# Kernel tuning notes

Measured on AMD Instinct MI355X. Metric: run time of the kernel, lower is better.

## Reference

```python
import jax, jax.numpy as jnp
import numpy as np

N, D, H, O, P = 50000, 256, 512, 64, 1024


def setup_inputs() -> dict:
    key = jax.random.key(0)
    ks = jax.random.split(key, 9)
    x = jax.random.normal(ks[0], (N, D), dtype=jnp.float32)
    W1 = jax.random.normal(ks[1], (H, D), dtype=jnp.float32) / np.sqrt(D)
    b1 = jax.random.normal(ks[2], (H,), dtype=jnp.float32) * 0.01
    W2 = jax.random.normal(ks[3], (O, H), dtype=jnp.float32) / np.sqrt(H)
    b2 = jax.random.normal(ks[4], (O,), dtype=jnp.float32) * 0.01
    ap = jax.random.randint(ks[5], (P,), 0, N, dtype=jnp.int32)
    p = jax.random.randint(ks[6], (P,), 0, N, dtype=jnp.int32)
    an = jax.random.randint(ks[7], (P,), 0, N, dtype=jnp.int32)
    n = jax.random.randint(ks[8], (P,), 0, N, dtype=jnp.int32)
    return {"x": x, "W1": W1, "b1": b1, "W2": W2, "b2": b2,
            "ap": ap, "p": p, "an": an, "n": n}


def reference(x, W1, b1, W2, b2, ap, p, an, n):
    """ContrastiveHessianCalculator.compute_hessian, loss_func='contrastive_full',
    wrt='weight', shape='diagonal', speed='half' (exact GGN diag), for the nnj net
    Linear(D,H) -> Tanh -> Linear(H,O).

    For a pair (x1,x2) the combined diag m0 - 2*m1 + m2 equals
    diag((J1-J2)^T (J1-J2)) where Ji = d f(xi)/d params. Closed form per layer:
      W1[i,j]: S11_i*x1_j^2 - 2*S12_i*x1_j*x2_j + S22_i*x2_j^2,
               Sab_i = tanh'(z1a)_i * tanh'(z1b)_i * sum_o W2[o,i]^2
      b1[i]:   S11_i - 2*S12_i + S22_i
      W2[i,j]: (h1_j - h2_j)^2  (independent of output row i)
      b2[i]:   0  (bias Jacobians of the two branches cancel)
    Per-layer diags are flattened [weight, bias] and concatenated (torch.cat(.., dim=1)),
    then summed over the pair batch; return sum(pos) - sum(neg).
    """
    c = jnp.sum(W2 * W2, axis=0)  # [H]

    def pair_hess_diag(ia, ib):
        xa = x[ia]            # [P, D]
        xb = x[ib]            # [P, D]
        ha = jnp.tanh(xa @ W1.T + b1)   # [P, H]
        hb = jnp.tanh(xb @ W1.T + b1)
        da = 1.0 - ha * ha              # tanh' at x_a, [P, H]
        db = 1.0 - hb * hb
        S11 = da * da * c               # [P, H]
        S12 = da * db * c
        S22 = db * db * c
        # W1 diag: [P, H, D]
        W1d = (S11[:, :, None] * (xa * xa)[:, None, :]
               - 2.0 * S12[:, :, None] * (xa * xb)[:, None, :]
               + S22[:, :, None] * (xb * xb)[:, None, :])
        b1d = S11 - 2.0 * S12 + S22      # [P, H]
        hd = (ha - hb) ** 2              # [P, H]
        W2d = jnp.broadcast_to(hd[:, None, :], (hd.shape[0], O, H))  # [P, O, H]
        b2d = jnp.zeros((hd.shape[0], O), dtype=hd.dtype)
        flat = jnp.concatenate([W1d.reshape(hd.shape[0], -1), b1d,
                                W2d.reshape(hd.shape[0], -1), b2d], axis=1)
        return jnp.sum(flat, axis=0)     # sum over pair batch -> [n_params]

    pos = pair_hess_diag(ap, p)
    neg = pair_hess_diag(an, n)
    return pos - neg
```

## Files before the change

kernel.cpp:

```cpp
#include <hip/hip_runtime.h>
#include <math.h>

#define DD_ 256
#define HH_ 512
#define OO_ 64

typedef __attribute__((ext_vector_type(8))) short bf16x8s;
typedef __attribute__((ext_vector_type(4))) float f32x4;

__device__ __forceinline__ unsigned short f2bf(float f) {
    unsigned u = __float_as_uint(f);
    u += 0x7FFF + ((u >> 16) & 1);
    return (unsigned short)(u >> 16);
}
__device__ __forceinline__ float bf2f(unsigned short h) {
    return __uint_as_float(((unsigned)h) << 16);
}
__device__ __forceinline__ int swz4(int r, int g) {
    return g ^ (r & 3) ^ ((r >> 2) & 3);
}

__global__ __launch_bounds__(256) void k_mega(
    const float* __restrict__ x, const float* __restrict__ W1,
    const float* __restrict__ b1, const float* __restrict__ W2,
    const int* __restrict__ ap, const int* __restrict__ pI,
    const int* __restrict__ an, const int* __restrict__ nI,
    short* __restrict__ Mt, short* __restrict__ Xt,
    float* __restrict__ pb1, float* __restrict__ phd) {
    const int t = threadIdx.x;
    const int bb = blockIdx.x;
    if (bb < 512) {
        __shared__ short Ah[64 * 32], Al[64 * 32], Bh[64 * 32], Bl[64 * 32];
        __shared__ float ht[64][67];
        __shared__ int sidx[64];
        const int n0 = (bb & 7) * 64;
        const int ry = bb >> 3;
        const int s = ry >> 5;
        const int p0 = (ry & 31) * 32;
        const int* IA = s ? an : ap;
        const int* IB = s ? nI : pI;
        if (t < 32) sidx[t] = IA[p0 + t];
        else if (t < 64) sidx[t] = IB[p0 + t - 32];
        __syncthreads();
        const int row = t >> 2, q = t & 3;
        const int l = t & 63, w = t >> 6;
        const int wm = w >> 1, wn = w & 1;
        const int lm = l & 15, g = l >> 4;
        const int sw = swz4(row, q);
        f32x4 acc[2][2] = {};
        for (int k0 = 0; k0 < DD_; k0 += 32) {
            {
                const float* src = x + (size_t)sidx[row] * DD_ + k0 + q * 8;
                float4 v0 = *(const float4*)src;
                float4 v1 = *(const float4*)(src + 4);
                float f[8] = {v0.x, v0.y, v0.z, v0.w, v1.x, v1.y, v1.z, v1.w};
                bf16x8s hi, lo;
                #pragma unroll
                for (int e = 0; e < 8; ++e) {
                    unsigned short hh = f2bf(f[e]);
                    hi[e] = (short)hh;
                    lo[e] = (short)f2bf(f[e] - bf2f(hh));
                }
                *(bf16x8s*)(&Ah[(row * 4 + sw) * 8]) = hi;
                *(bf16x8s*)(&Al[(row * 4 + sw) * 8]) = lo;
            }
            {
                const float* src = W1 + (size_t)(n0 + row) * DD_ + k0 + q * 8;
                float4 v0 = *(const float4*)src;
                float4 v1 = *(const float4*)(src + 4);
                float f[8] = {v0.x, v0.y, v0.z, v0.w, v1.x, v1.y, v1.z, v1.w};
                bf16x8s hi, lo;
                #pragma unroll
                for (int e = 0; e < 8; ++e) {
                    unsigned short hh = f2bf(f[e]);
                    hi[e] = (short)hh;
                    lo[e] = (short)f2bf(f[e] - bf2f(hh));
                }
                *(bf16x8s*)(&Bh[(row * 4 + sw) * 8]) = hi;
                *(bf16x8s*)(&Bl[(row * 4 + sw) * 8]) = lo;
            }
            __syncthreads();
            bf16x8s ah[2], al[2], bh[2], bl[2];
            #pragma unroll
            for (int mi = 0; mi < 2; ++mi) {
                int r = wm * 32 + mi * 16 + lm;
                ah[mi] = *(const bf16x8s*)(&Ah[(r * 4 + swz4(r, g)) * 8]);
                al[mi] = *(const bf16x8s*)(&Al[(r * 4 + swz4(r, g)) * 8]);
            }
            #pragma unroll
            for (int nj = 0; nj < 2; ++nj) {
                int r = wn * 32 + nj * 16 + lm;
                bh[nj] = *(const bf16x8s*)(&Bh[(r * 4 + swz4(r, g)) * 8]);
                bl[nj] = *(const bf16x8s*)(&Bl[(r * 4 + swz4(r, g)) * 8]);
            }
            #pragma unroll
            for (int mi = 0; mi < 2; ++mi)
                #pragma unroll
                for (int nj = 0; nj < 2; ++nj) {
                    acc[mi][nj] = __builtin_amdgcn_mfma_f32_16x16x32_bf16(ah[mi], bh[nj], acc[mi][nj], 0, 0, 0);
                    acc[mi][nj] = __builtin_amdgcn_mfma_f32_16x16x32_bf16(ah[mi], bl[nj], acc[mi][nj], 0, 0, 0);
                    acc[mi][nj] = __builtin_amdgcn_mfma_f32_16x16x32_bf16(al[mi], bh[nj], acc[mi][nj], 0, 0, 0);
                }
            __syncthreads();
        }
        #pragma unroll
        for (int mi = 0; mi < 2; ++mi)
            #pragma unroll
            for (int nj = 0; nj < 2; ++nj) {
                int jl = wn * 32 + nj * 16 + lm;
                float bv = b1[n0 + jl];
                #pragma unroll
                for (int qq = 0; qq < 4; ++qq) {
                    int r = wm * 32 + mi * 16 + g * 4 + qq;
                    ht[r][jl] = tanhf(acc[mi][nj][qq] + bv);
                }
            }
        __syncthreads();
        const int il = t >> 2, pq = t & 3;
        float ci = 0.f;
        #pragma unroll 8
        for (int o = 0; o < OO_; ++o) { float wv = W2[o * HH_ + n0 + il]; ci += wv * wv; }
        const float sgn = s ? -1.f : 1.f;
        float b1p = 0.f, hdp = 0.f;
        bf16x8s v0, v1, v2;
        #pragma unroll
        for (int pp = 0; pp < 8; ++pp) {
            int pl = pq * 8 + pp;
            float ha = ht[pl][il];
            float hb = ht[pl + 32][il];
            float da = 1.f - ha * ha, db = 1.f - hb * hb;
            float s11 = sgn * (da * da * ci);
            float s12 = sgn * (-2.f * da * db * ci);
            float s22 = sgn * (db * db * ci);
            v0[pp] = (short)f2bf(s11);
            v1[pp] = (short)f2bf(s12);
            v2[pp] = (short)f2bf(s22);
            b1p += s11 + s12 + s22;
            float d = ha - hb;
            hdp += sgn * d * d;
        }
        size_t base = (size_t)(n0 + il) * 6144 + s * 1024 + p0 + pq * 8;
        *(bf16x8s*)(&Mt[base]) = v0;
        *(bf16x8s*)(&Mt[base + 2048]) = v1;
        *(bf16x8s*)(&Mt[base + 4096]) = v2;
        b1p += __shfl_xor(b1p, 1); b1p += __shfl_xor(b1p, 2);
        hdp += __shfl_xor(hdp, 1); hdp += __shfl_xor(hdp, 2);
        if (pq == 0) { pb1[ry * HH_ + n0 + il] = b1p; phd[ry * HH_ + n0 + il] = hdp; }
    } else {
        __shared__ int sia[64], sib[64];
        const int b2 = bb - 512;
        const int jblk = b2 >> 5, pblk = b2 & 31;
        const int j = jblk * 64 + (t >> 2), pq = t & 3;
        const int p0 = pblk * 64;
        const int s = p0 >> 10;
        const int* IA = s ? an : ap;
        const int* IB = s ? nI : pI;
        if (t < 64) sia[t] = IA[(p0 & 1023) + t];
        else if (t < 128) sib[t - 64] = IB[(p0 & 1023) + (t - 64)];
        __syncthreads();
        short xv[3][16];
        #pragma unroll
        for (int pp = 0; pp < 16; ++pp) {
            int pl = pq * 16 + pp;
            float xa = x[(size_t)sia[pl] * DD_ + j];
            float xb = x[(size_t)sib[pl] * DD_ + j];
            xv[0][pp] = (short)f2bf(xa * xa);
            xv[1][pp] = (short)f2bf(xa * xb);
            xv[2][pp] = (short)f2bf(xb * xb);
        }
        size_t base = (size_t)j * 6144 + p0 + pq * 16;
        #pragma unroll
        for (int term = 0; term < 3; ++term) {
            bf16x8s v0, v1;
            #pragma unroll
            for (int e = 0; e < 8; ++e) { v0[e] = xv[term][e]; v1[e] = xv[term][e + 8]; }
            *(bf16x8s*)(&Xt[base + (size_t)term * 2048]) = v0;
            *(bf16x8s*)(&Xt[base + (size_t)term * 2048 + 8]) = v1;
        }
    }
}

__global__ __launch_bounds__(256) void k_gemm2(
    const short* __restrict__ Mt, const short* __restrict__ Xt,
    float* __restrict__ part) {
    __shared__ short As[64 * 32], Bs[64 * 32];
    const int t = threadIdx.x;
    const int j0 = blockIdx.x * 64;
    const int i0 = blockIdx.y * 64;
    const int kb = blockIdx.z;
    const int row = t >> 2, q = t & 3;
    const int l = t & 63, w = t >> 6;
    const int wm = w >> 1, wn = w & 1;
    const int lm = l & 15, g = l >> 4;
    const int sw = swz4(row, q);
    f32x4 acc[2][2] = {};
    for (int ks = 0; ks < 12; ++ks) {
        const int k0 = kb * 384 + ks * 32;
        *(bf16x8s*)(&As[(row * 4 + sw) * 8]) =
            *(const bf16x8s*)(&Mt[(size_t)(i0 + row) * 6144 + k0 + q * 8]);
        *(bf16x8s*)(&Bs[(row * 4 + sw) * 8]) =
            *(const bf16x8s*)(&Xt[(size_t)(j0 + row) * 6144 + k0 + q * 8]);
        __syncthreads();
        bf16x8s a[2], b[2];
        #pragma unroll
        for (int mi = 0; mi < 2; ++mi) {
            int r = wm * 32 + mi * 16 + lm;
            a[mi] = *(const bf16x8s*)(&As[(r * 4 + swz4(r, g)) * 8]);
        }
        #pragma unroll
        for (int nj = 0; nj < 2; ++nj) {
            int r = wn * 32 + nj * 16 + lm;
            b[nj] = *(const bf16x8s*)(&Bs[(r * 4 + swz4(r, g)) * 8]);
        }
        #pragma unroll
        for (int mi = 0; mi < 2; ++mi)
            #pragma unroll
            for (int nj = 0; nj < 2; ++nj)
                acc[mi][nj] = __builtin_amdgcn_mfma_f32_16x16x32_bf16(a[mi], b[nj], acc[mi][nj], 0, 0, 0);
        __syncthreads();
    }
    #pragma unroll
    for (int mi = 0; mi < 2; ++mi)
        #pragma unroll
        for (int nj = 0; nj < 2; ++nj) {
            int j = j0 + wn * 32 + nj * 16 + lm;
            #pragma unroll
            for (int qq = 0; qq < 4; ++qq) {
                int i = i0 + wm * 32 + mi * 16 + g * 4 + qq;
                part[((size_t)kb * HH_ + i) * DD_ + j] = acc[mi][nj][qq];
            }
        }
}

__global__ void k_tail(const float* __restrict__ part, const float* __restrict__ pb1,
                       const float* __restrict__ phd, float* __restrict__ out) {
    int gid = blockIdx.x * 256 + threadIdx.x;
    const int HD = HH_ * DD_;
    if (gid < HD) {
        float sv = 0.f;
        #pragma unroll
        for (int kb = 0; kb < 16; ++kb) sv += part[(size_t)kb * HD + gid];
        out[gid] = sv;
    } else if (gid < HD + HH_) {
        int i = gid - HD;
        float sv = 0.f;
        #pragma unroll
        for (int kb = 0; kb < 64; ++kb) sv += pb1[kb * HH_ + i];
        out[gid] = sv;
    } else if (gid < HD + HH_ + OO_ * HH_) {
        int i = (gid - HD - HH_) & (HH_ - 1);
        float sv = 0.f;
        #pragma unroll
        for (int kb = 0; kb < 64; ++kb) sv += phd[kb * HH_ + i];
        out[gid] = sv;
    } else if (gid < HD + HH_ + OO_ * HH_ + OO_) {
        out[gid] = 0.f;
    }
}

extern "C" void kernel_launch(void* const* d_in, const int* in_sizes, int n_in,
                              void* d_out, int out_size, void* d_ws, size_t ws_size,
                              hipStream_t stream) {
    const float* x  = (const float*)d_in[0];
    const float* W1 = (const float*)d_in[1];
    const float* b1 = (const float*)d_in[2];
    const float* W2 = (const float*)d_in[3];
    const int* ap = (const int*)d_in[5];
    const int* pI = (const int*)d_in[6];
    const int* an = (const int*)d_in[7];
    const int* nI = (const int*)d_in[8];
    float* out = (float*)d_out;
    float* ws = (float*)d_ws;

    float* part = ws;
    short* Mt   = (short*)(ws + 2097152);
    short* Xt   = (short*)(ws + 3670016);
    float* pb1  = ws + 4456448;
    float* phd  = ws + 4489216;

    k_mega<<<dim3(640), dim3(256), 0, stream>>>(x, W1, b1, W2, ap, pI, an, nI,
                                                Mt, Xt, pb1, phd);
    k_gemm2<<<dim3(4, 8, 16), dim3(256), 0, stream>>>(Mt, Xt, part);
    k_tail<<<dim3(643), dim3(256), 0, stream>>>(part, pb1, phd, out);
}
```

Before: 33.20 us.

## Fuse split-K reduction into GEMM via last-block election, merge Xt build into mega blocks

Removes the separate tail kernel by having the last arriving split-K block per output tile (tracked with atomic counters) sum the 16 partials and write the output. Block (0,0,0) also handles the bias and W2-diagonal reductions. The Xt construction blocks are folded into the 512 GEMM1 blocks, so every block does both tasks and the grid shrinks from 640. This adds a memset launch, atomics, and a serialized reduction on the final block of each tile.

```diff
diff --git a/kernel.cpp b/kernel.cpp
--- a/kernel.cpp
+++ b/kernel.cpp
@@ -6,6 +6,7 @@
 #define OO_ 64
 
 typedef __attribute__((ext_vector_type(8))) short bf16x8s;
+typedef __attribute__((ext_vector_type(4))) short bf16x4s;
 typedef __attribute__((ext_vector_type(4))) float f32x4;
 
 __device__ __forceinline__ unsigned short f2bf(float f) {
@@ -27,95 +28,95 @@
     const int* __restrict__ an, const int* __restrict__ nI,
     short* __restrict__ Mt, short* __restrict__ Xt,
     float* __restrict__ pb1, float* __restrict__ phd) {
+    __shared__ short Ah[64 * 32], Al[64 * 32], Bh[64 * 32], Bl[64 * 32];
+    __shared__ float ht[64][67];
+    __shared__ int sidx[64];
     const int t = threadIdx.x;
     const int bb = blockIdx.x;
-    if (bb < 512) {
-        __shared__ short Ah[64 * 32], Al[64 * 32], Bh[64 * 32], Bl[64 * 32];
-        __shared__ float ht[64][67];
-        __shared__ int sidx[64];
-        const int n0 = (bb & 7) * 64;
-        const int ry = bb >> 3;
-        const int s = ry >> 5;
-        const int p0 = (ry & 31) * 32;
-        const int* IA = s ? an : ap;
-        const int* IB = s ? nI : pI;
-        if (t < 32) sidx[t] = IA[p0 + t];
-        else if (t < 64) sidx[t] = IB[p0 + t - 32];
+    const int n0 = (bb & 7) * 64;
+    const int ry = bb >> 3;
+    const int s = ry >> 5;
+    const int p0 = (ry & 31) * 32;
+    const int* IA = s ? an : ap;
+    const int* IB = s ? nI : pI;
+    if (t < 32) sidx[t] = IA[p0 + t];
+    else if (t < 64) sidx[t] = IB[p0 + t - 32];
+    __syncthreads();
+    const int row = t >> 2, q = t & 3;
+    const int l = t & 63, w = t >> 6;
+    const int wm = w >> 1, wn = w & 1;
+    const int lm = l & 15, g = l >> 4;
+    const int sw = swz4(row, q);
+    f32x4 acc[2][2] = {};
+    for (int k0 = 0; k0 < DD_; k0 += 32) {
+        {
+            const float* src = x + (size_t)sidx[row] * DD_ + k0 + q * 8;
+            float4 v0 = *(const float4*)src;
+            float4 v1 = *(const float4*)(src + 4);
+            float f[8] = {v0.x, v0.y, v0.z, v0.w, v1.x, v1.y, v1.z, v1.w};
+            bf16x8s hi, lo;
+            #pragma unroll
+            for (int e = 0; e < 8; ++e) {
+                unsigned short hh = f2bf(f[e]);
+                hi[e] = (short)hh;
+                lo[e] = (short)f2bf(f[e] - bf2f(hh));
+            }
+            *(bf16x8s*)(&Ah[(row * 4 + sw) * 8]) = hi;
+            *(bf16x8s*)(&Al[(row * 4 + sw) * 8]) = lo;
+        }
+        {
+            const float* src = W1 + (size_t)(n0 + row) * DD_ + k0 + q * 8;
+            float4 v0 = *(const float4*)src;
+            float4 v1 = *(const float4*)(src + 4);
+            float f[8] = {v0.x, v0.y, v0.z, v0.w, v1.x, v1.y, v1.z, v1.w};
+            bf16x8s hi, lo;
+            #pragma unroll
+            for (int e = 0; e < 8; ++e) {
+                unsigned short hh = f2bf(f[e]);
+                hi[e] = (short)hh;
+                lo[e] = (short)f2bf(f[e] - bf2f(hh));
+            }
+            *(bf16x8s*)(&Bh[(row * 4 + sw) * 8]) = hi;
+            *(bf16x8s*)(&Bl[(row * 4 + sw) * 8]) = lo;
+        }
         __syncthreads();
-        const int row = t >> 2, q = t & 3;
-        const int l = t & 63, w = t >> 6;
-        const int wm = w >> 1, wn = w & 1;
-        const int lm = l & 15, g = l >> 4;
-        const int sw = swz4(row, q);
-        f32x4 acc[2][2] = {};
-        for (int k0 = 0; k0 < DD_; k0 += 32) {
-            {
-                const float* src = x + (size_t)sidx[row] * DD_ + k0 + q * 8;
-                float4 v0 = *(const float4*)src;
-                float4 v1 = *(const float4*)(src + 4);
-                float f[8] = {v0.x, v0.y, v0.z, v0.w, v1.x, v1.y, v1.z, v1.w};
-                bf16x8s hi, lo;
-                #pragma unroll
-                for (int e = 0; e < 8; ++e) {
-                    unsigned short hh = f2bf(f[e]);
-                    hi[e] = (short)hh;
-                    lo[e] = (short)f2bf(f[e] - bf2f(hh));
-                }
-                *(bf16x8s*)(&Ah[(row * 4 + sw) * 8]) = hi;
-                *(bf16x8s*)(&Al[(row * 4 + sw) * 8]) = lo;
-            }
-            {
-                const float* src = W1 + (size_t)(n0 + row) * DD_ + k0 + q * 8;
-                float4 v0 = *(const float4*)src;
-                float4 v1 = *(const float4*)(src + 4);
-                float f[8] = {v0.x, v0.y, v0.z, v0.w, v1.x, v1.y, v1.z, v1.w};
-                bf16x8s hi, lo;
-                #pragma unroll
-                for (int e = 0; e < 8; ++e) {
-                    unsigned short hh = f2bf(f[e]);
-                    hi[e] = (short)hh;
-                    lo[e] = (short)f2bf(f[e] - bf2f(hh));
-                }
-                *(bf16x8s*)(&Bh[(row * 4 + sw) * 8]) = hi;
-                *(bf16x8s*)(&Bl[(row * 4 + sw) * 8]) = lo;
-            }
-            __syncthreads();
-            bf16x8s ah[2], al[2], bh[2], bl[2];
-            #pragma unroll
-            for (int mi = 0; mi < 2; ++mi) {
-                int r = wm * 32 + mi * 16 + lm;
-                ah[mi] = *(const bf16x8s*)(&Ah[(r * 4 + swz4(r, g)) * 8]);
-                al[mi] = *(const bf16x8s*)(&Al[(r * 4 + swz4(r, g)) * 8]);
-            }
+        bf16x8s ah[2], al[2], bh[2], bl[2];
+        #pragma unroll
+        for (int mi = 0; mi < 2; ++mi) {
+            int r = wm * 32 + mi * 16 + lm;
+            ah[mi] = *(const bf16x8s*)(&Ah[(r * 4 + swz4(r, g)) * 8]);
+            al[mi] = *(const bf16x8s*)(&Al[(r * 4 + swz4(r, g)) * 8]);
+        }
+        #pragma unroll
+        for (int nj = 0; nj < 2; ++nj) {
+            int r = wn * 32 + nj * 16 + lm;
+            bh[nj] = *(const bf16x8s*)(&Bh[(r * 4 + swz4(r, g)) * 8]);
+            bl[nj] = *(const bf16x8s*)(&Bl[(r * 4 + swz4(r, g)) * 8]);
+        }
+        #pragma unroll
+        for (int mi = 0; mi < 2; ++mi)
             #pragma unroll
             for (int nj = 0; nj < 2; ++nj) {
-                int r = wn * 32 + nj * 16 + lm;
-                bh[nj] = *(const bf16x8s*)(&Bh[(r * 4 + swz4(r, g)) * 8]);
-                bl[nj] = *(const bf16x8s*)(&Bl[(r * 4 + swz4(r, g)) * 8]);
-            }
-            #pragma unroll
-            for (int mi = 0; mi < 2; ++mi)
-                #pragma unroll
-                for (int nj = 0; nj < 2; ++nj) {
-                    acc[mi][nj] = __builtin_amdgcn_mfma_f32_16x16x32_bf16(ah[mi], bh[nj], acc[mi][nj], 0, 0, 0);
-                    acc[mi][nj] = __builtin_amdgcn_mfma_f32_16x16x32_bf16(ah[mi], bl[nj], acc[mi][nj], 0, 0, 0);
-                    acc[mi][nj] = __builtin_amdgcn_mfma_f32_16x16x32_bf16(al[mi], bh[nj], acc[mi][nj], 0, 0, 0);
-                }
-            __syncthreads();
-        }
-        #pragma unroll
-        for (int mi = 0; mi < 2; ++mi)
-            #pragma unroll
-            for (int nj = 0; nj < 2; ++nj) {
-                int jl = wn * 32 + nj * 16 + lm;
-                float bv = b1[n0 + jl];
-                #pragma unroll
-                for (int qq = 0; qq < 4; ++qq) {
-                    int r = wm * 32 + mi * 16 + g * 4 + qq;
-                    ht[r][jl] = tanhf(acc[mi][nj][qq] + bv);
-                }
+                acc[mi][nj] = __builtin_amdgcn_mfma_f32_16x16x32_bf16(ah[mi], bh[nj], acc[mi][nj], 0, 0, 0);
+                acc[mi][nj] = __builtin_amdgcn_mfma_f32_16x16x32_bf16(ah[mi], bl[nj], acc[mi][nj], 0, 0, 0);
+                acc[mi][nj] = __builtin_amdgcn_mfma_f32_16x16x32_bf16(al[mi], bh[nj], acc[mi][nj], 0, 0, 0);
             }
         __syncthreads();
+    }
+    #pragma unroll
+    for (int mi = 0; mi < 2; ++mi)
+        #pragma unroll
+        for (int nj = 0; nj < 2; ++nj) {
+            int jl = wn * 32 + nj * 16 + lm;
+            float bv = b1[n0 + jl];
+            #pragma unroll
+            for (int qq = 0; qq < 4; ++qq) {
+                int r = wm * 32 + mi * 16 + g * 4 + qq;
+                ht[r][jl] = tanhf(acc[mi][nj][qq] + bv);
+            }
+        }
+    __syncthreads();
+    {
         const int il = t >> 2, pq = t & 3;
         float ci = 0.f;
         #pragma unroll 8
@@ -146,48 +147,67 @@
         b1p += __shfl_xor(b1p, 1); b1p += __shfl_xor(b1p, 2);
         hdp += __shfl_xor(hdp, 1); hdp += __shfl_xor(hdp, 2);
         if (pq == 0) { pb1[ry * HH_ + n0 + il] = b1p; phd[ry * HH_ + n0 + il] = hdp; }
-    } else {
-        __shared__ int sia[64], sib[64];
-        const int b2 = bb - 512;
-        const int jblk = b2 >> 5, pblk = b2 & 31;
-        const int j = jblk * 64 + (t >> 2), pq = t & 3;
-        const int p0 = pblk * 64;
-        const int s = p0 >> 10;
-        const int* IA = s ? an : ap;
-        const int* IB = s ? nI : pI;
-        if (t < 64) sia[t] = IA[(p0 & 1023) + t];
-        else if (t < 128) sib[t - 64] = IB[(p0 & 1023) + (t - 64)];
-        __syncthreads();
-        short xv[3][16];
-        #pragma unroll
-        for (int pp = 0; pp < 16; ++pp) {
-            int pl = pq * 16 + pp;
-            float xa = x[(size_t)sia[pl] * DD_ + j];
-            float xb = x[(size_t)sib[pl] * DD_ + j];
+    }
+    {
+        const int xb = bb >> 2;
+        const int quarter = bb & 3;
+        const int jblk = xb >> 5, pblk = xb & 31;
+        const int j = jblk * 64 + (t >> 2);
+        const int pq = t & 3;
+        const int p0x = pblk * 64;
+        const int sX = p0x >> 10;
+        const int* IA2 = sX ? an : ap;
+        const int* IB2 = sX ? nI : pI;
+        const int pbase = (p0x & 1023) + quarter * 16 + pq * 4;
+        short xv[3][4];
+        #pragma unroll
+        for (int pp = 0; pp < 4; ++pp) {
+            int ia = IA2[pbase + pp];
+            int ib = IB2[pbase + pp];
+            float xa = x[(size_t)ia * DD_ + j];
+            float xbv = x[(size_t)ib * DD_ + j];
             xv[0][pp] = (short)f2bf(xa * xa);
-            xv[1][pp] = (short)f2bf(xa * xb);
-            xv[2][pp] = (short)f2bf(xb * xb);
-        }
-        size_t base = (size_t)j * 6144 + p0 + pq * 16;
+            xv[1][pp] = (short)f2bf(xa * xbv);
+            xv[2][pp] = (short)f2bf(xbv * xbv);
+        }
+        size_t base = (size_t)j * 6144 + p0x + quarter * 16 + pq * 4;
         #pragma unroll
         for (int term = 0; term < 3; ++term) {
-            bf16x8s v0, v1;
-            #pragma unroll
-            for (int e = 0; e < 8; ++e) { v0[e] = xv[term][e]; v1[e] = xv[term][e + 8]; }
-            *(bf16x8s*)(&Xt[base + (size_t)term * 2048]) = v0;
-            *(bf16x8s*)(&Xt[base + (size_t)term * 2048 + 8]) = v1;
-        }
-    }
-}
-
-__global__ __launch_bounds__(256) void k_gemm2(
+            bf16x4s v;
+            #pragma unroll
+            for (int e = 0; e < 4; ++e) v[e] = xv[term][e];
+            *(bf16x4s*)(&Xt[base + (size_t)term * 2048]) = v;
+        }
+    }
+}
+
+__global__ __launch_bounds__(256) void k_gemm2f(
     const short* __restrict__ Mt, const short* __restrict__ Xt,
-    float* __restrict__ part) {
+    float* __restrict__ part, const float* __restrict__ pb1,
+    const float* __restrict__ phd, float* __restrict__ out,
+    int* __restrict__ counters) {
     __shared__ short As[64 * 32], Bs[64 * 32];
+    __shared__ int elected;
     const int t = threadIdx.x;
-    const int j0 = blockIdx.x * 64;
-    const int i0 = blockIdx.y * 64;
-    const int kb = blockIdx.z;
+    const int bx = blockIdx.x, by = blockIdx.y, kb = blockIdx.z;
+    const int j0 = bx * 64;
+    const int i0 = by * 64;
+    const int HD = HH_ * DD_;
+    if (bx == 0 && by == 0 && kb == 0) {
+        const int i2 = t * 2;
+        float s0 = 0.f, s1 = 0.f, h0 = 0.f, h1 = 0.f;
+        for (int k2 = 0; k2 < 64; ++k2) {
+            float2 pv = *(const float2*)(&pb1[k2 * HH_ + i2]);
+            float2 hv = *(const float2*)(&phd[k2 * HH_ + i2]);
+            s0 += pv.x; s1 += pv.y; h0 += hv.x; h1 += hv.y;
+        }
+        *(float2*)(&out[HD + i2]) = make_float2(s0, s1);
+        float2 hb2 = make_float2(h0, h1);
+        #pragma unroll 4
+        for (int o = 0; o < OO_; ++o)
+            *(float2*)(&out[HD + HH_ + o * HH_ + i2]) = hb2;
+        if (t < OO_) out[HD + HH_ + OO_ * HH_ + t] = 0.f;
+    }
     const int row = t >> 2, q = t & 3;
     const int l = t & 63, w = t >> 6;
     const int wm = w >> 1, wn = w & 1;
@@ -230,31 +250,27 @@
                 part[((size_t)kb * HH_ + i) * DD_ + j] = acc[mi][nj][qq];
             }
         }
-}
-
-__global__ void k_tail(const float* __restrict__ part, const float* __restrict__ pb1,
-                       const float* __restrict__ phd, float* __restrict__ out) {
-    int gid = blockIdx.x * 256 + threadIdx.x;
-    const int HD = HH_ * DD_;
-    if (gid < HD) {
-        float sv = 0.f;
-        #pragma unroll
-        for (int kb = 0; kb < 16; ++kb) sv += part[(size_t)kb * HD + gid];
-        out[gid] = sv;
-    } else if (gid < HD + HH_) {
-        int i = gid - HD;
-        float sv = 0.f;
-        #pragma unroll
-        for (int kb = 0; kb < 64; ++kb) sv += pb1[kb * HH_ + i];
-        out[gid] = sv;
-    } else if (gid < HD + HH_ + OO_ * HH_) {
-        int i = (gid - HD - HH_) & (HH_ - 1);
-        float sv = 0.f;
-        #pragma unroll
-        for (int kb = 0; kb < 64; ++kb) sv += phd[kb * HH_ + i];
-        out[gid] = sv;
-    } else if (gid < HD + HH_ + OO_ * HH_ + OO_) {
-        out[gid] = 0.f;
+    __threadfence();
+    __syncthreads();
+    if (t == 0) elected = (atomicAdd(&counters[by * 4 + bx], 1) == 15);
+    __syncthreads();
+    if (elected) {
+        __threadfence();
+        const int il = t >> 2;
+        const int jc = (t & 3) * 16;
+        f32x4 sum[4] = {};
+        for (int k2 = 0; k2 < 16; ++k2) {
+            const float* p = &part[((size_t)k2 * HH_ + i0 + il) * DD_ + j0 + jc];
+            #pragma unroll
+            for (int cc = 0; cc < 4; ++cc) {
+                f32x4 v = *(const f32x4*)(p + cc * 4);
+                sum[cc] += v;
+            }
+        }
+        float* o = &out[(size_t)(i0 + il) * DD_ + j0 + jc];
+        #pragma unroll
+        for (int cc = 0; cc < 4; ++cc)
+            *(f32x4*)(o + cc * 4) = sum[cc];
     }
 }
 
@@ -277,9 +293,11 @@
     short* Xt   = (short*)(ws + 3670016);
     float* pb1  = ws + 4456448;
     float* phd  = ws + 4489216;
-
-    k_mega<<<dim3(640), dim3(256), 0, stream>>>(x, W1, b1, W2, ap, pI, an, nI,
+    int* counters = (int*)(ws + 4521984);
+
+    hipMemsetAsync(counters, 0, 32 * sizeof(int), stream);
+    k_mega<<<dim3(512), dim3(256), 0, stream>>>(x, W1, b1, W2, ap, pI, an, nI,
                                                 Mt, Xt, pb1, phd);
-    k_gemm2<<<dim3(4, 8, 16), dim3(256), 0, stream>>>(Mt, Xt, part);
-    k_tail<<<dim3(643), dim3(256), 0, stream>>>(part, pb1, phd, out);
-}
+    k_gemm2f<<<dim3(4, 8, 16), dim3(256), 0, stream>>>(Mt, Xt, part, pb1, phd,
+                                                       out, counters);
+}
```

New measurement: 102.9 us. +210.1%, slower.

## Prefetch next k-tile into registers, use fast tanh, vectorize tail reduction

Applied to the files above, without the earlier changes.

Both GEMM loops now load the next k-slice from global memory into registers right after the barrier, so the load latency overlaps the MFMA work on the current tile. The tanh in the first layer is replaced by an exp-based fast approximation. The tail kernel is vectorized to float4 and computes each W2-diagonal column sum once before writing it to all 64 rows, which cuts the grid from 643 to 130 blocks. The fast tanh trades a small loss of accuracy for cheaper math.

```diff
diff --git a/kernel.cpp b/kernel.cpp
--- a/kernel.cpp
+++ b/kernel.cpp
@@ -18,6 +18,10 @@
 }
 __device__ __forceinline__ int swz4(int r, int g) {
     return g ^ (r & 3) ^ ((r >> 2) & 3);
+}
+__device__ __forceinline__ float fast_tanh(float z) {
+    float e = __expf(2.f * z);
+    return 1.f - __fdividef(2.f, e + 1.f);
 }
 
 __global__ __launch_bounds__(256) void k_mega(
@@ -47,13 +51,16 @@
         const int wm = w >> 1, wn = w & 1;
         const int lm = l & 15, g = l >> 4;
         const int sw = swz4(row, q);
+        const float* srcA = x + (size_t)sidx[row] * DD_ + q * 8;
+        const float* srcB = W1 + (size_t)(n0 + row) * DD_ + q * 8;
+        float4 pa0 = *(const float4*)srcA;
+        float4 pa1 = *(const float4*)(srcA + 4);
+        float4 pb0 = *(const float4*)srcB;
+        float4 pb1v = *(const float4*)(srcB + 4);
         f32x4 acc[2][2] = {};
         for (int k0 = 0; k0 < DD_; k0 += 32) {
             {
-                const float* src = x + (size_t)sidx[row] * DD_ + k0 + q * 8;
-                float4 v0 = *(const float4*)src;
-                float4 v1 = *(const float4*)(src + 4);
-                float f[8] = {v0.x, v0.y, v0.z, v0.w, v1.x, v1.y, v1.z, v1.w};
+                float f[8] = {pa0.x, pa0.y, pa0.z, pa0.w, pa1.x, pa1.y, pa1.z, pa1.w};
                 bf16x8s hi, lo;
                 #pragma unroll
                 for (int e = 0; e < 8; ++e) {
@@ -65,10 +72,7 @@
                 *(bf16x8s*)(&Al[(row * 4 + sw) * 8]) = lo;
             }
             {
-                const float* src = W1 + (size_t)(n0 + row) * DD_ + k0 + q * 8;
-                float4 v0 = *(const float4*)src;
-                float4 v1 = *(const float4*)(src + 4);
-                float f[8] = {v0.x, v0.y, v0.z, v0.w, v1.x, v1.y, v1.z, v1.w};
+                float f[8] = {pb0.x, pb0.y, pb0.z, pb0.w, pb1v.x, pb1v.y, pb1v.z, pb1v.w};
                 bf16x8s hi, lo;
                 #pragma unroll
                 for (int e = 0; e < 8; ++e) {
@@ -80,6 +84,12 @@
                 *(bf16x8s*)(&Bl[(row * 4 + sw) * 8]) = lo;
             }
             __syncthreads();
+            if (k0 + 32 < DD_) {
+                pa0 = *(const float4*)(srcA + k0 + 32);
+                pa1 = *(const float4*)(srcA + k0 + 36);
+                pb0 = *(const float4*)(srcB + k0 + 32);
+                pb1v = *(const float4*)(srcB + k0 + 36);
+            }
             bf16x8s ah[2], al[2], bh[2], bl[2];
             #pragma unroll
             for (int mi = 0; mi < 2; ++mi) {
@@ -112,7 +122,7 @@
                 #pragma unroll
                 for (int qq = 0; qq < 4; ++qq) {
                     int r = wm * 32 + mi * 16 + g * 4 + qq;
-                    ht[r][jl] = tanhf(acc[mi][nj][qq] + bv);
+                    ht[r][jl] = fast_tanh(acc[mi][nj][qq] + bv);
                 }
             }
         __syncthreads();
@@ -193,14 +203,19 @@
     const int wm = w >> 1, wn = w & 1;
     const int lm = l & 15, g = l >> 4;
     const int sw = swz4(row, q);
+    const short* srcA = &Mt[(size_t)(i0 + row) * 6144 + kb * 384 + q * 8];
+    const short* srcB = &Xt[(size_t)(j0 + row) * 6144 + kb * 384 + q * 8];
+    bf16x8s ra = *(const bf16x8s*)srcA;
+    bf16x8s rb = *(const bf16x8s*)srcB;
     f32x4 acc[2][2] = {};
     for (int ks = 0; ks < 12; ++ks) {
-        const int k0 = kb * 384 + ks * 32;
-        *(bf16x8s*)(&As[(row * 4 + sw) * 8]) =
-            *(const bf16x8s*)(&Mt[(size_t)(i0 + row) * 6144 + k0 + q * 8]);
-        *(bf16x8s*)(&Bs[(row * 4 + sw) * 8]) =
-            *(const bf16x8s*)(&Xt[(size_t)(j0 + row) * 6144 + k0 + q * 8]);
-        __syncthreads();
+        *(bf16x8s*)(&As[(row * 4 + sw) * 8]) = ra;
+        *(bf16x8s*)(&Bs[(row * 4 + sw) * 8]) = rb;
+        __syncthreads();
+        if (ks < 11) {
+            ra = *(const bf16x8s*)(srcA + (ks + 1) * 32);
+            rb = *(const bf16x8s*)(srcB + (ks + 1) * 32);
+        }
         bf16x8s a[2], b[2];
         #pragma unroll
         for (int mi = 0; mi < 2; ++mi) {
@@ -234,27 +249,32 @@
 
 __global__ void k_tail(const float* __restrict__ part, const float* __restrict__ pb1,
                        const float* __restrict__ phd, float* __restrict__ out) {
-    int gid = blockIdx.x * 256 + threadIdx.x;
-    const int HD = HH_ * DD_;
-    if (gid < HD) {
-        float sv = 0.f;
-        #pragma unroll
-        for (int kb = 0; kb < 16; ++kb) sv += part[(size_t)kb * HD + gid];
-        out[gid] = sv;
-    } else if (gid < HD + HH_) {
-        int i = gid - HD;
-        float sv = 0.f;
-        #pragma unroll
-        for (int kb = 0; kb < 64; ++kb) sv += pb1[kb * HH_ + i];
-        out[gid] = sv;
-    } else if (gid < HD + HH_ + OO_ * HH_) {
-        int i = (gid - HD - HH_) & (HH_ - 1);
-        float sv = 0.f;
-        #pragma unroll
-        for (int kb = 0; kb < 64; ++kb) sv += phd[kb * HH_ + i];
-        out[gid] = sv;
-    } else if (gid < HD + HH_ + OO_ * HH_ + OO_) {
-        out[gid] = 0.f;
+    const int gid = blockIdx.x * 256 + threadIdx.x;
+    const int HD4 = 32768;
+    f32x4* out4 = (f32x4*)out;
+    if (gid < HD4) {
+        f32x4 sv = {};
+        #pragma unroll
+        for (int kb = 0; kb < 16; ++kb)
+            sv += *(const f32x4*)(&part[(size_t)kb * 131072 + gid * 4]);
+        out4[gid] = sv;
+    } else if (gid < HD4 + 128) {
+        const int i4 = gid - HD4;
+        f32x4 sv = {};
+        for (int k2 = 0; k2 < 64; ++k2)
+            sv += *(const f32x4*)(&pb1[k2 * HH_ + i4 * 4]);
+        out4[HD4 + i4] = sv;
+    } else if (gid < HD4 + 256) {
+        const int i4 = gid - HD4 - 128;
+        f32x4 sv = {};
+        for (int k2 = 0; k2 < 64; ++k2)
+            sv += *(const f32x4*)(&phd[k2 * HH_ + i4 * 4]);
+        #pragma unroll 8
+        for (int o = 0; o < OO_; ++o)
+            out4[HD4 + 128 + o * 128 + i4] = sv;
+    } else if (gid < HD4 + 272) {
+        f32x4 z = {};
+        out4[41088 + gid - HD4 - 256] = z;
     }
 }
 
@@ -281,5 +301,5 @@
     k_mega<<<dim3(640), dim3(256), 0, stream>>>(x, W1, b1, W2, ap, pI, an, nI,
                                                 Mt, Xt, pb1, phd);
     k_gemm2<<<dim3(4, 8, 16), dim3(256), 0, stream>>>(Mt, Xt, part);
-    k_tail<<<dim3(643), dim3(256), 0, stream>>>(part, pb1, phd, out);
-}
+    k_tail<<<dim3(130), dim3(256), 0, stream>>>(part, pb1, phd, out);
+}
```

Measured after the change: 33.81 us. No clear change (+1.9%).
